# Optimization experiments

Hardware: AMD Instinct MI355X
Metric: run time of the kernel (lower is better)

## Reference

```python
import jax, jax.numpy as jnp
import numpy as np

B, C, H, W = 32, 128, 56, 56
O = 256
KH, KW = 3, 3
SH, SW = 1, 1
PH, PW = 1, 1
T = 6          # num_terms
R = 8          # low_rank
D = C * KH * KW          # 1152
R2 = R * KH * KW         # 72


def setup_inputs() -> dict:
    key = jax.random.key(0)
    ks = jax.random.split(key, 6)
    scale = 0.05
    return {
        "x": jax.random.normal(ks[0], (B, C, H, W), dtype=jnp.float32),
        "S1s": jax.random.normal(ks[1], (T, D, R), dtype=jnp.float32) * scale,
        "U1s": jax.random.normal(ks[2], (T, R, O), dtype=jnp.float32) * scale,
        "U2s": jax.random.normal(ks[3], (T, R2, D), dtype=jnp.float32) * scale,
        "S2s": jax.random.normal(ks[4], (T, R2, O), dtype=jnp.float32) * scale,
        "bias": jax.random.normal(ks[5], (O,), dtype=jnp.float32) * scale,
    }


def _extract_windows(x):
    # im2col: pad then gather strided windows; d flattened in (C, kh, kw) order
    xp = jnp.pad(x, ((0, 0), (0, 0), (PH, PH), (PW, PW)))
    Hp, Wp = xp.shape[2], xp.shape[3]
    Ho = (Hp - KH) // SH + 1
    Wo = (Wp - KW) // SW + 1
    # stack KH*KW shifted views -> [B, C, KH*KW, Ho, Wo]
    patches = jnp.stack(
        [xp[:, :, i:i + SH * Ho:SH, j:j + SW * Wo:SW]
         for i in range(KH) for j in range(KW)],
        axis=2,
    )
    # -> [B, Ho, Wo, C, KH*KW] -> [N, C*KH*KW]
    xw = patches.transpose(0, 3, 4, 1, 2).reshape(B * Ho * Wo, D)
    return xw, Ho, Wo


def reference(x, S1s, U1s, U2s, S2s, bias):
    xw, Ho, Wo = _extract_windows(x)                    # [N, D]
    # term 1: x_windows @ S1s[t] @ U1s[t], averaged over terms
    out1 = jnp.einsum('nd,tdr,tro->no', xw, S1s, U1s, optimize=True) / T + bias
    # term 2: x_windows @ U2s[t].T @ S2s[t], averaged over terms
    out2 = jnp.einsum('nd,tdr,tro->no', xw, jnp.swapaxes(U2s, 1, 2), S2s,
                      optimize=True) / T
    # NOTE: bias is added twice, faithfully matching the original module
    out = (out1 + out2 + bias).reshape(B, Ho, Wo, O).transpose(0, 3, 1, 2)
    return out
```

## Files before the change

kernel.cpp:

```cpp
#include <hip/hip_runtime.h>
#include <hip/hip_bf16.h>

typedef __attribute__((ext_vector_type(8))) short  short8;
typedef __attribute__((ext_vector_type(8))) unsigned short ushort8;
typedef __attribute__((ext_vector_type(4))) unsigned short usv4;
typedef __attribute__((ext_vector_type(4))) float  f32x4;

#define D_DIM 1152
#define O_DIM 256
#define N_TOT 100352
#define XT_H 58
#define XT_ROW (58 * 128)

__device__ __forceinline__ unsigned short f2bf(float f) {
  __hip_bfloat16 h = __float2bfloat16(f);
  return __builtin_bit_cast(unsigned short, h);
}

#define GLOAD_LDS16(g, l)                                              \
  __builtin_amdgcn_global_load_lds(                                    \
      (const __attribute__((address_space(1))) void*)(g),              \
      (__attribute__((address_space(3))) void*)(l), 16, 0, 0)

__global__ __launch_bounds__(256) void wt_kernel(
    const float* __restrict__ S1s, const float* __restrict__ U1s,
    const float* __restrict__ U2s, const float* __restrict__ S2s,
    unsigned short* __restrict__ Wt) {
  __shared__ float A_lds[32][64];
  __shared__ float B_lds[32][64];

  const int bo = blockIdx.x & 3;
  const int bd = blockIdx.x >> 2;
  const int o0  = bo << 6;
  const int dn0 = bd << 6;
  const int rr  = dn0 >> 7;
  const int c0  = dn0 & 127;

  const int tid = threadIdx.x;
  const int ty = tid >> 4, tx = tid & 15;

  float acc[4][4] = {};

  for (int kc = 0; kc < 15; ++kc) {
#pragma unroll
    for (int e = 0; e < 8; ++e) {
      const int li = e * 256 + tid;
      const int kk = li >> 6;
      const int xx = li & 63;
      const int k  = kc * 32 + kk;
      float av, bv;
      if (k < 48) {
        av = U1s[k * O_DIM + o0 + xx];
        const int d_old = (c0 + xx) * 9 + rr;
        bv = S1s[(size_t)((k >> 3) * D_DIM + d_old) * 8 + (k & 7)];
      } else {
        const int kq = k - 48;
        av = S2s[(size_t)kq * O_DIM + o0 + xx];
        const int d_old = (c0 + xx) * 9 + rr;
        bv = U2s[(size_t)kq * D_DIM + d_old];
      }
      A_lds[kk][xx] = av;
      B_lds[kk][xx] = bv;
    }
    __syncthreads();
#pragma unroll
    for (int kk = 0; kk < 32; ++kk) {
      f32x4 a = *(const f32x4*)&A_lds[kk][ty << 2];
      f32x4 b = *(const f32x4*)&B_lds[kk][tx << 2];
#pragma unroll
      for (int i = 0; i < 4; ++i)
#pragma unroll
        for (int j = 0; j < 4; ++j)
          acc[i][j] += a[i] * b[j];
    }
    __syncthreads();
  }

#pragma unroll
  for (int i = 0; i < 4; ++i) {
    usv4 v;
#pragma unroll
    for (int j = 0; j < 4; ++j) v[j] = f2bf(acc[i][j] * (1.0f / 6.0f));
    *(usv4*)(Wt + (size_t)(o0 + (ty << 2) + i) * D_DIM + dn0 + (tx << 2)) = v;
  }
}

__global__ __launch_bounds__(256) void pad_kernel(const float* __restrict__ x,
                                                  unsigned short* __restrict__ xt) {
  int blk = blockIdx.x;
  int b = blk / XT_H, ih = blk - b * XT_H;
  unsigned short* dst = xt + (size_t)blk * XT_ROW;
  int tid = threadIdx.x;

  if (ih == 0 || ih == XT_H - 1) {
    ushort8 z;
#pragma unroll
    for (int q = 0; q < 8; ++q) z[q] = 0;
    for (int i = tid; i < XT_ROW / 8; i += 256) ((ushort8*)dst)[i] = z;
    return;
  }

  __shared__ unsigned short lds[128 * 58];
  int h = ih - 1;
  const float* xb = x + (size_t)b * 128 * 3136 + (size_t)h * 56;
#pragma unroll 4
  for (int r = 0; r < 28; ++r) {
    int idx = r * 256 + tid;
    int c = idx / 56, w2 = idx - c * 56;
    lds[c * 58 + w2] = f2bf(xb[(size_t)c * 3136 + w2]);
  }
  __syncthreads();
#pragma unroll 4
  for (int r = 0; r < 29; ++r) {
    int idx = r * 256 + tid;
    int iw = idx >> 7, c = idx & 127;
    unsigned short v = 0;
    if (iw >= 1 && iw <= 56) v = lds[c * 58 + (iw - 1)];
    dst[idx] = v;
  }
}

#define ABYTE(bf_, ks_) ((bf_) * 65536 + (ks_) * 16384)
#define BBYTE(bf_, ks_) ((bf_) * 65536 + 32768 + (ks_) * 16384)

__device__ __forceinline__ constexpr int KOF(int kt) {
  int rr = kt >> 1;
  return ((rr / 3) * 58 + (rr % 3)) * 128 + (kt & 1) * 64;
}

#define STAGE(kt_, ks_, bf_) do {                                              \
  GLOAD_LDS16(pA0 + (kt_) * 64 + (ks_) * 32,                                   \
              smem + (ABYTE(bf_, ks_) >> 1) + stoff0);                         \
  GLOAD_LDS16(pA1 + (kt_) * 64 + (ks_) * 32,                                   \
              smem + (ABYTE(bf_, ks_) >> 1) + stoff1);                         \
  GLOAD_LDS16(pB0 + KOF(kt_) + (ks_) * 32,                                     \
              smem + (BBYTE(bf_, ks_) >> 1) + stoff0);                         \
  GLOAD_LDS16(pB1 + KOF(kt_) + (ks_) * 32,                                     \
              smem + (BBYTE(bf_, ks_) >> 1) + stoff1);                         \
} while (0)

__global__ __launch_bounds__(512, 2) void gemm_kernel(
    const unsigned short* __restrict__ Wt, const unsigned short* __restrict__ xt,
    const float* __restrict__ bias, float* __restrict__ out) {
  __shared__ __align__(1024) unsigned short smem[65536];

  const int bid   = blockIdx.x;
  const int ntile = (bid & 7) * 49 + (bid >> 3);
  const int n0    = ntile << 8;

  const int tid  = threadIdx.x;
  const int w    = tid >> 6;
  const int lane = tid & 63;
  const int wm   = w >> 2;
  const int wn   = w & 3;

  const int stoff0 = w << 9;
  const int stoff1 = 4096 + (w << 9);

  const unsigned short *pA0, *pA1, *pB0, *pB1;
  {
    const int li0 = tid, li1 = 512 + tid;
    const int r0 = li0 >> 2, g0 = (li0 & 3) ^ (r0 & 3);
    const int r1 = li1 >> 2, g1 = (li1 & 3) ^ (r1 & 3);
    pA0 = Wt + (size_t)r0 * D_DIM + g0 * 8;
    pA1 = Wt + (size_t)r1 * D_DIM + g1 * 8;
    int n_g0 = n0 + r0;
    int b0 = n_g0 / 3136, s0 = n_g0 - b0 * 3136;
    int oh0 = s0 / 56, ow0 = s0 - oh0 * 56;
    pB0 = xt + (((size_t)b0 * XT_H + oh0) * XT_H + ow0) * 128 + g0 * 8;
    int n_g1 = n0 + r1;
    int b1 = n_g1 / 3136, s1 = n_g1 - b1 * 3136;
    int oh1 = s1 / 56, ow1 = s1 - oh1 * 56;
    pB1 = xt + (((size_t)b1 * XT_H + oh1) * XT_H + ow1) * 128 + g1 * 8;
  }

  f32x4 acc[8][4] = {};

  const int la15 = lane & 15;
  const int frq  = (((lane >> 4) ^ (lane & 3)) << 4);

  STAGE(0, 0, 0);
  STAGE(0, 1, 0);
  STAGE(1, 0, 1);
  asm volatile("s_waitcnt vmcnt(8)" ::: "memory");
  __builtin_amdgcn_s_barrier();

#pragma unroll
  for (int kt = 0; kt < 18; ++kt) {
    const int bsel = kt & 1;
#pragma unroll
    for (int p = 0; p < 2; ++p) {
      const char* Abase = (const char*)smem + ABYTE(bsel, p);
      const char* Bbase = (const char*)smem + BBYTE(bsel, p);

      short8 af[8], bfr[4];
#pragma unroll
      for (int mi = 0; mi < 8; ++mi)
        af[mi] = *(const short8*)(Abase + ((wm << 7) + (mi << 4) + la15) * 64 + frq);
#pragma unroll
      for (int ni = 0; ni < 4; ++ni)
        bfr[ni] = *(const short8*)(Bbase + ((wn << 6) + (ni << 4) + la15) * 64 + frq);

      if (p == 0) {
        if (kt + 1 < 18) STAGE(kt + 1, 1, (kt + 1) & 1);
      } else {
        if (kt + 2 < 18) STAGE(kt + 2, 0, kt & 1);
      }
      __builtin_amdgcn_s_barrier();

      __builtin_amdgcn_s_setprio(1);
#pragma unroll
      for (int mi = 0; mi < 8; ++mi)
#pragma unroll
        for (int ni = 0; ni < 4; ++ni)
          acc[mi][ni] = __builtin_amdgcn_mfma_f32_16x16x32_bf16(
              af[mi], bfr[ni], acc[mi][ni], 0, 0, 0);
      __builtin_amdgcn_s_setprio(0);

      if (kt < 16 || (kt == 16 && p == 0))
        asm volatile("s_waitcnt vmcnt(8)" ::: "memory");
      else if (kt == 16)
        asm volatile("s_waitcnt vmcnt(4)" ::: "memory");
      else if (kt == 17 && p == 0)
        asm volatile("s_waitcnt vmcnt(0)" ::: "memory");
      __builtin_amdgcn_s_barrier();
    }
  }

  const int lr = (lane >> 4) << 2;
#pragma unroll
  for (int ni = 0; ni < 4; ++ni) {
    const int ng = n0 + (wn << 6) + (ni << 4) + la15;
    const int b  = ng / 3136;
    const int s  = ng - b * 3136;
    float* op = out + (size_t)b * (O_DIM * 3136) + s;
#pragma unroll
    for (int mi = 0; mi < 8; ++mi) {
      const int og = (wm << 7) + (mi << 4) + lr;
#pragma unroll
      for (int r = 0; r < 4; ++r)
        op[(size_t)(og + r) * 3136] = acc[mi][ni][r] + 2.0f * bias[og + r];
    }
  }
}

extern "C" void kernel_launch(void* const* d_in, const int* in_sizes, int n_in,
                              void* d_out, int out_size, void* d_ws, size_t ws_size,
                              hipStream_t stream) {
  const float* x    = (const float*)d_in[0];
  const float* S1s  = (const float*)d_in[1];
  const float* U1s  = (const float*)d_in[2];
  const float* U2s  = (const float*)d_in[3];
  const float* S2s  = (const float*)d_in[4];
  const float* bias = (const float*)d_in[5];
  float* out = (float*)d_out;
  (void)ws_size;

  unsigned short* xt = (unsigned short*)d_ws;
  unsigned short* Wt = (unsigned short*)((char*)d_ws + (size_t)32 * XT_H * XT_ROW * 2);

  pad_kernel<<<dim3(32 * XT_H), dim3(256), 0, stream>>>(x, xt);
  wt_kernel<<<dim3(72), dim3(256), 0, stream>>>(S1s, U1s, U2s, S2s, Wt);
  gemm_kernel<<<dim3(392), dim3(512), 0, stream>>>(Wt, xt, bias, out);
}
```

Before: 134.4 us.

## Restructure GEMM mainloop into four-phase ping-pong with 64-wide K tiles

```diff
diff --git a/kernel.cpp b/kernel.cpp
--- a/kernel.cpp
+++ b/kernel.cpp
@@ -120,26 +120,37 @@
   }
 }
 
-#define ABYTE(bf_, ks_) ((bf_) * 65536 + (ks_) * 16384)
-#define BBYTE(bf_, ks_) ((bf_) * 65536 + 32768 + (ks_) * 16384)
-
 __device__ __forceinline__ constexpr int KOF(int kt) {
   int rr = kt >> 1;
   return ((rr / 3) * 58 + (rr % 3)) * 128 + (kt & 1) * 64;
 }
 
-#define STAGE(kt_, ks_, bf_) do {                                              \
-  GLOAD_LDS16(pA0 + (kt_) * 64 + (ks_) * 32,                                   \
-              smem + (ABYTE(bf_, ks_) >> 1) + stoff0);                         \
-  GLOAD_LDS16(pA1 + (kt_) * 64 + (ks_) * 32,                                   \
-              smem + (ABYTE(bf_, ks_) >> 1) + stoff1);                         \
-  GLOAD_LDS16(pB0 + KOF(kt_) + (ks_) * 32,                                     \
-              smem + (BBYTE(bf_, ks_) >> 1) + stoff0);                         \
-  GLOAD_LDS16(pB1 + KOF(kt_) + (ks_) * 32,                                     \
-              smem + (BBYTE(bf_, ks_) >> 1) + stoff1);                         \
+#define ST_A(kt_, bf_) do {                                                    \
+  GLOAD_LDS16(pA0 + (kt_) * 64,                  smem + (bf_) * 32768 + tid * 8);          \
+  GLOAD_LDS16(pA0 + (kt_) * 64 +  64 * D_DIM,    smem + (bf_) * 32768 + 4096 + tid * 8);   \
+  GLOAD_LDS16(pA0 + (kt_) * 64 + 128 * D_DIM,    smem + (bf_) * 32768 + 8192 + tid * 8);   \
+  GLOAD_LDS16(pA0 + (kt_) * 64 + 192 * D_DIM,    smem + (bf_) * 32768 + 12288 + tid * 8);  \
 } while (0)
-
-__global__ __launch_bounds__(512, 2) void gemm_kernel(
+#define ST_B(kt_, bf_) do {                                                    \
+  GLOAD_LDS16(pB[0] + KOF(kt_), smem + (bf_) * 32768 + 16384 + tid * 8);       \
+  GLOAD_LDS16(pB[1] + KOF(kt_), smem + (bf_) * 32768 + 20480 + tid * 8);       \
+  GLOAD_LDS16(pB[2] + KOF(kt_), smem + (bf_) * 32768 + 24576 + tid * 8);       \
+  GLOAD_LDS16(pB[3] + KOF(kt_), smem + (bf_) * 32768 + 28672 + tid * 8);       \
+} while (0)
+
+#define AFRAG(bf_, row, ks)                                                    \
+  (*(const short8*)((const char*)smem + (bf_) * 65536 + (row) * 128 +          \
+      (((((ks) << 2) + (lane >> 4)) ^ ((row) & 7)) << 4)))
+#define BFRAG(bf_, row, ks)                                                    \
+  (*(const short8*)((const char*)smem + (bf_) * 65536 + 32768 + (row) * 128 +  \
+      (((((ks) << 2) + (lane >> 4)) ^ ((row) & 7)) << 4)))
+
+#define PHASE_BAR() do {                                                       \
+  __builtin_amdgcn_s_barrier();                                                \
+  asm volatile("s_waitcnt lgkmcnt(0)" ::: "memory");                           \
+} while (0)
+
+__global__ __launch_bounds__(512, 1) void gemm_kernel(
     const unsigned short* __restrict__ Wt, const unsigned short* __restrict__ xt,
     const float* __restrict__ bias, float* __restrict__ out) {
   __shared__ __align__(1024) unsigned short smem[65536];
@@ -153,78 +164,99 @@
   const int lane = tid & 63;
   const int wm   = w >> 2;
   const int wn   = w & 3;
-
-  const int stoff0 = w << 9;
-  const int stoff1 = 4096 + (w << 9);
-
-  const unsigned short *pA0, *pA1, *pB0, *pB1;
-  {
-    const int li0 = tid, li1 = 512 + tid;
-    const int r0 = li0 >> 2, g0 = (li0 & 3) ^ (r0 & 3);
-    const int r1 = li1 >> 2, g1 = (li1 & 3) ^ (r1 & 3);
-    pA0 = Wt + (size_t)r0 * D_DIM + g0 * 8;
-    pA1 = Wt + (size_t)r1 * D_DIM + g1 * 8;
-    int n_g0 = n0 + r0;
-    int b0 = n_g0 / 3136, s0 = n_g0 - b0 * 3136;
-    int oh0 = s0 / 56, ow0 = s0 - oh0 * 56;
-    pB0 = xt + (((size_t)b0 * XT_H + oh0) * XT_H + ow0) * 128 + g0 * 8;
-    int n_g1 = n0 + r1;
-    int b1 = n_g1 / 3136, s1 = n_g1 - b1 * 3136;
-    int oh1 = s1 / 56, ow1 = s1 - oh1 * 56;
-    pB1 = xt + (((size_t)b1 * XT_H + oh1) * XT_H + ow1) * 128 + g1 * 8;
+  const int la15 = lane & 15;
+
+  const int srow = tid >> 3;
+  const int sg   = (tid & 7) ^ (srow & 7);
+  const unsigned short* pA0 = Wt + (size_t)srow * D_DIM + sg * 8;
+  const unsigned short* pB[4];
+#pragma unroll
+  for (int r = 0; r < 4; ++r) {
+    const int n_g = n0 + r * 64 + srow;
+    const int b   = n_g / 3136;
+    const int s   = n_g - b * 3136;
+    const int oh  = s / 56, ow = s - oh * 56;
+    pB[r] = xt + (((size_t)b * XT_H + oh) * XT_H + ow) * 128 + sg * 8;
   }
 
   f32x4 acc[8][4] = {};
-
-  const int la15 = lane & 15;
-  const int frq  = (((lane >> 4) ^ (lane & 3)) << 4);
-
-  STAGE(0, 0, 0);
-  STAGE(0, 1, 0);
-  STAGE(1, 0, 1);
-  asm volatile("s_waitcnt vmcnt(8)" ::: "memory");
+  short8 afr[4], bfr[4];
+
+  ST_A(0, 0);
+  ST_B(0, 0);
+  asm volatile("s_waitcnt vmcnt(0)" ::: "memory");
   __builtin_amdgcn_s_barrier();
 
 #pragma unroll
   for (int kt = 0; kt < 18; ++kt) {
-    const int bsel = kt & 1;
-#pragma unroll
-    for (int p = 0; p < 2; ++p) {
-      const char* Abase = (const char*)smem + ABYTE(bsel, p);
-      const char* Bbase = (const char*)smem + BBYTE(bsel, p);
-
-      short8 af[8], bfr[4];
-#pragma unroll
-      for (int mi = 0; mi < 8; ++mi)
-        af[mi] = *(const short8*)(Abase + ((wm << 7) + (mi << 4) + la15) * 64 + frq);
-#pragma unroll
-      for (int ni = 0; ni < 4; ++ni)
-        bfr[ni] = *(const short8*)(Bbase + ((wn << 6) + (ni << 4) + la15) * 64 + frq);
-
-      if (p == 0) {
-        if (kt + 1 < 18) STAGE(kt + 1, 1, (kt + 1) & 1);
-      } else {
-        if (kt + 2 < 18) STAGE(kt + 2, 0, kt & 1);
-      }
-      __builtin_amdgcn_s_barrier();
-
-      __builtin_amdgcn_s_setprio(1);
-#pragma unroll
-      for (int mi = 0; mi < 8; ++mi)
-#pragma unroll
-        for (int ni = 0; ni < 4; ++ni)
-          acc[mi][ni] = __builtin_amdgcn_mfma_f32_16x16x32_bf16(
-              af[mi], bfr[ni], acc[mi][ni], 0, 0, 0);
-      __builtin_amdgcn_s_setprio(0);
-
-      if (kt < 16 || (kt == 16 && p == 0))
-        asm volatile("s_waitcnt vmcnt(8)" ::: "memory");
-      else if (kt == 16)
-        asm volatile("s_waitcnt vmcnt(4)" ::: "memory");
-      else if (kt == 17 && p == 0)
-        asm volatile("s_waitcnt vmcnt(0)" ::: "memory");
-      __builtin_amdgcn_s_barrier();
-    }
+    const int bf = kt & 1;
+    const int nb = bf ^ 1;
+    const bool more = (kt + 1) < 18;
+
+#pragma unroll
+    for (int mi = 0; mi < 4; ++mi)
+      afr[mi] = AFRAG(bf, (wm << 7) + (mi << 4) + la15, 0);
+#pragma unroll
+    for (int ni = 0; ni < 4; ++ni)
+      bfr[ni] = BFRAG(bf, (wn << 6) + (ni << 4) + la15, 0);
+    if (more) ST_A(kt + 1, nb);
+    PHASE_BAR();
+    __builtin_amdgcn_s_setprio(1);
+#pragma unroll
+    for (int mi = 0; mi < 4; ++mi)
+#pragma unroll
+      for (int ni = 0; ni < 4; ++ni)
+        acc[mi][ni] = __builtin_amdgcn_mfma_f32_16x16x32_bf16(
+            afr[mi], bfr[ni], acc[mi][ni], 0, 0, 0);
+    __builtin_amdgcn_s_setprio(0);
+    __builtin_amdgcn_s_barrier();
+
+#pragma unroll
+    for (int mi = 0; mi < 4; ++mi)
+      afr[mi] = AFRAG(bf, (wm << 7) + ((mi + 4) << 4) + la15, 0);
+    if (more) ST_B(kt + 1, nb);
+    PHASE_BAR();
+    __builtin_amdgcn_s_setprio(1);
+#pragma unroll
+    for (int mi = 0; mi < 4; ++mi)
+#pragma unroll
+      for (int ni = 0; ni < 4; ++ni)
+        acc[4 + mi][ni] = __builtin_amdgcn_mfma_f32_16x16x32_bf16(
+            afr[mi], bfr[ni], acc[4 + mi][ni], 0, 0, 0);
+    __builtin_amdgcn_s_setprio(0);
+    __builtin_amdgcn_s_barrier();
+
+#pragma unroll
+    for (int mi = 0; mi < 4; ++mi)
+      afr[mi] = AFRAG(bf, (wm << 7) + (mi << 4) + la15, 1);
+#pragma unroll
+    for (int ni = 0; ni < 4; ++ni)
+      bfr[ni] = BFRAG(bf, (wn << 6) + (ni << 4) + la15, 1);
+    PHASE_BAR();
+    __builtin_amdgcn_s_setprio(1);
+#pragma unroll
+    for (int mi = 0; mi < 4; ++mi)
+#pragma unroll
+      for (int ni = 0; ni < 4; ++ni)
+        acc[mi][ni] = __builtin_amdgcn_mfma_f32_16x16x32_bf16(
+            afr[mi], bfr[ni], acc[mi][ni], 0, 0, 0);
+    __builtin_amdgcn_s_setprio(0);
+    __builtin_amdgcn_s_barrier();
+
+#pragma unroll
+    for (int mi = 0; mi < 4; ++mi)
+      afr[mi] = AFRAG(bf, (wm << 7) + ((mi + 4) << 4) + la15, 1);
+    PHASE_BAR();
+    __builtin_amdgcn_s_setprio(1);
+#pragma unroll
+    for (int mi = 0; mi < 4; ++mi)
+#pragma unroll
+      for (int ni = 0; ni < 4; ++ni)
+        acc[4 + mi][ni] = __builtin_amdgcn_mfma_f32_16x16x32_bf16(
+            afr[mi], bfr[ni], acc[4 + mi][ni], 0, 0, 0);
+    __builtin_amdgcn_s_setprio(0);
+    asm volatile("s_waitcnt vmcnt(0)" ::: "memory");
+    __builtin_amdgcn_s_barrier();
   }
 
   const int lr = (lane >> 4) << 2;
```

Result: faster. 126.7 us (-5.7%).

## Restructure GEMM main loop into a four-slot LDS ring with one barrier per step

Applied to the files above, without the earlier changes.

```diff
diff --git a/kernel.cpp b/kernel.cpp
--- a/kernel.cpp
+++ b/kernel.cpp
@@ -120,26 +120,28 @@
   }
 }
 
-#define ABYTE(bf_, ks_) ((bf_) * 65536 + (ks_) * 16384)
-#define BBYTE(bf_, ks_) ((bf_) * 65536 + 32768 + (ks_) * 16384)
-
 __device__ __forceinline__ constexpr int KOF(int kt) {
   int rr = kt >> 1;
   return ((rr / 3) * 58 + (rr % 3)) * 128 + (kt & 1) * 64;
 }
 
-#define STAGE(kt_, ks_, bf_) do {                                              \
-  GLOAD_LDS16(pA0 + (kt_) * 64 + (ks_) * 32,                                   \
-              smem + (ABYTE(bf_, ks_) >> 1) + stoff0);                         \
-  GLOAD_LDS16(pA1 + (kt_) * 64 + (ks_) * 32,                                   \
-              smem + (ABYTE(bf_, ks_) >> 1) + stoff1);                         \
-  GLOAD_LDS16(pB0 + KOF(kt_) + (ks_) * 32,                                     \
-              smem + (BBYTE(bf_, ks_) >> 1) + stoff0);                         \
-  GLOAD_LDS16(pB1 + KOF(kt_) + (ks_) * 32,                                     \
-              smem + (BBYTE(bf_, ks_) >> 1) + stoff1);                         \
+#define STAGE_S(s_) do {                                                       \
+  GLOAD_LDS16(pA0 + (s_) * 32, smem + ((s_) & 3) * 16384 + (tid << 3));        \
+  GLOAD_LDS16(pA1 + (s_) * 32, smem + ((s_) & 3) * 16384 + 4096 + (tid << 3)); \
+  GLOAD_LDS16(pB0 + KOF((s_) >> 1) + ((s_) & 1) * 32,                          \
+              smem + ((s_) & 3) * 16384 + 8192 + (tid << 3));                  \
+  GLOAD_LDS16(pB1 + KOF((s_) >> 1) + ((s_) & 1) * 32,                          \
+              smem + ((s_) & 3) * 16384 + 12288 + (tid << 3));                 \
 } while (0)
 
-__global__ __launch_bounds__(512, 2) void gemm_kernel(
+#define AFRAG(q_, row_)                                                        \
+  (*(const short8*)((const char*)smem + (q_) * 32768 + (row_) * 64 +          \
+      ((((lane >> 4) ^ (((row_) >> 1) & 3)) << 4))))
+#define BFRAG(q_, row_)                                                        \
+  (*(const short8*)((const char*)smem + (q_) * 32768 + 16384 + (row_) * 64 +  \
+      ((((lane >> 4) ^ (((row_) >> 1) & 3)) << 4))))
+
+__global__ __launch_bounds__(512, 1) void gemm_kernel(
     const unsigned short* __restrict__ Wt, const unsigned short* __restrict__ xt,
     const float* __restrict__ bias, float* __restrict__ out) {
   __shared__ __align__(1024) unsigned short smem[65536];
@@ -149,82 +151,64 @@
   const int n0    = ntile << 8;
 
   const int tid  = threadIdx.x;
+  const int lane = tid & 63;
   const int w    = tid >> 6;
-  const int lane = tid & 63;
   const int wm   = w >> 2;
   const int wn   = w & 3;
-
-  const int stoff0 = w << 9;
-  const int stoff1 = 4096 + (w << 9);
-
-  const unsigned short *pA0, *pA1, *pB0, *pB1;
+  const int la15 = lane & 15;
+
+  const int srow = tid >> 2;
+  const int glog = (tid & 3) ^ ((tid >> 3) & 3);
+  const unsigned short* pA0 = Wt + (size_t)srow * D_DIM + glog * 8;
+  const unsigned short* pA1 = Wt + (size_t)(128 + srow) * D_DIM + glog * 8;
+  const unsigned short *pB0, *pB1;
   {
-    const int li0 = tid, li1 = 512 + tid;
-    const int r0 = li0 >> 2, g0 = (li0 & 3) ^ (r0 & 3);
-    const int r1 = li1 >> 2, g1 = (li1 & 3) ^ (r1 & 3);
-    pA0 = Wt + (size_t)r0 * D_DIM + g0 * 8;
-    pA1 = Wt + (size_t)r1 * D_DIM + g1 * 8;
-    int n_g0 = n0 + r0;
-    int b0 = n_g0 / 3136, s0 = n_g0 - b0 * 3136;
-    int oh0 = s0 / 56, ow0 = s0 - oh0 * 56;
-    pB0 = xt + (((size_t)b0 * XT_H + oh0) * XT_H + ow0) * 128 + g0 * 8;
-    int n_g1 = n0 + r1;
-    int b1 = n_g1 / 3136, s1 = n_g1 - b1 * 3136;
-    int oh1 = s1 / 56, ow1 = s1 - oh1 * 56;
-    pB1 = xt + (((size_t)b1 * XT_H + oh1) * XT_H + ow1) * 128 + g1 * 8;
+    int n_g = n0 + srow;
+    int b = n_g / 3136, s = n_g - b * 3136;
+    int oh = s / 56, ow = s - oh * 56;
+    pB0 = xt + (((size_t)b * XT_H + oh) * XT_H + ow) * 128 + glog * 8;
+    n_g = n0 + 128 + srow;
+    b = n_g / 3136; s = n_g - b * 3136;
+    oh = s / 56; ow = s - oh * 56;
+    pB1 = xt + (((size_t)b * XT_H + oh) * XT_H + ow) * 128 + glog * 8;
   }
 
   f32x4 acc[8][4] = {};
 
-  const int la15 = lane & 15;
-  const int frq  = (((lane >> 4) ^ (lane & 3)) << 4);
-
-  STAGE(0, 0, 0);
-  STAGE(0, 1, 0);
-  STAGE(1, 0, 1);
+  STAGE_S(0);
+  STAGE_S(1);
+  STAGE_S(2);
   asm volatile("s_waitcnt vmcnt(8)" ::: "memory");
   __builtin_amdgcn_s_barrier();
 
 #pragma unroll
-  for (int kt = 0; kt < 18; ++kt) {
-    const int bsel = kt & 1;
-#pragma unroll
-    for (int p = 0; p < 2; ++p) {
-      const char* Abase = (const char*)smem + ABYTE(bsel, p);
-      const char* Bbase = (const char*)smem + BBYTE(bsel, p);
-
-      short8 af[8], bfr[4];
-#pragma unroll
-      for (int mi = 0; mi < 8; ++mi)
-        af[mi] = *(const short8*)(Abase + ((wm << 7) + (mi << 4) + la15) * 64 + frq);
+  for (int s = 0; s < 36; ++s) {
+    const int q = s & 3;
+
+    short8 afr[8], bfr[4];
+#pragma unroll
+    for (int mi = 0; mi < 8; ++mi)
+      afr[mi] = AFRAG(q, (wm << 7) + (mi << 4) + la15);
+#pragma unroll
+    for (int ni = 0; ni < 4; ++ni)
+      bfr[ni] = BFRAG(q, (wn << 6) + (ni << 4) + la15);
+
+    if (s + 3 < 36) STAGE_S(s + 3);
+
+    if (s <= 32)      asm volatile("s_waitcnt vmcnt(8) lgkmcnt(0)" ::: "memory");
+    else if (s == 33) asm volatile("s_waitcnt vmcnt(4) lgkmcnt(0)" ::: "memory");
+    else              asm volatile("s_waitcnt vmcnt(0) lgkmcnt(0)" ::: "memory");
+    if (s < 35) __builtin_amdgcn_s_barrier();
+    __builtin_amdgcn_sched_barrier(0);
+
+    __builtin_amdgcn_s_setprio(1);
+#pragma unroll
+    for (int mi = 0; mi < 8; ++mi)
 #pragma unroll
       for (int ni = 0; ni < 4; ++ni)
-        bfr[ni] = *(const short8*)(Bbase + ((wn << 6) + (ni << 4) + la15) * 64 + frq);
-
-      if (p == 0) {
-        if (kt + 1 < 18) STAGE(kt + 1, 1, (kt + 1) & 1);
-      } else {
-        if (kt + 2 < 18) STAGE(kt + 2, 0, kt & 1);
-      }
-      __builtin_amdgcn_s_barrier();
-
-      __builtin_amdgcn_s_setprio(1);
-#pragma unroll
-      for (int mi = 0; mi < 8; ++mi)
-#pragma unroll
-        for (int ni = 0; ni < 4; ++ni)
-          acc[mi][ni] = __builtin_amdgcn_mfma_f32_16x16x32_bf16(
-              af[mi], bfr[ni], acc[mi][ni], 0, 0, 0);
-      __builtin_amdgcn_s_setprio(0);
-
-      if (kt < 16 || (kt == 16 && p == 0))
-        asm volatile("s_waitcnt vmcnt(8)" ::: "memory");
-      else if (kt == 16)
-        asm volatile("s_waitcnt vmcnt(4)" ::: "memory");
-      else if (kt == 17 && p == 0)
-        asm volatile("s_waitcnt vmcnt(0)" ::: "memory");
-      __builtin_amdgcn_s_barrier();
-    }
+        acc[mi][ni] = __builtin_amdgcn_mfma_f32_16x16x32_bf16(
+            afr[mi], bfr[ni], acc[mi][ni], 0, 0, 0);
+    __builtin_amdgcn_s_setprio(0);
   }
 
   const int lr = (lane >> 4) << 2;
```

Measured after the change: 122.2 us. -9.1%, faster.
